# Performance work log

Hardware: AMD Instinct MI355X
Metric: run time of the kernel (lower is better)

The kernel has to match this reference:

```python
import jax, jax.numpy as jnp
import numpy as np

BLOCK_SIZE = 256
EMB = 384
HEAD = 64
B = 256
T = 256

def setup_inputs() -> dict:
    key = jax.random.key(0)
    k1, k2, k3, k4 = jax.random.split(key, 4)
    x = jax.random.normal(k1, (B, T, EMB), dtype=jnp.float32)
    # torch Linear(no bias) default init ~ U(-1/sqrt(in), 1/sqrt(in)); use scaled normal
    s = 1.0 / np.sqrt(EMB)
    Wq = jax.random.normal(k2, (EMB, HEAD), dtype=jnp.float32) * s
    Wk = jax.random.normal(k3, (EMB, HEAD), dtype=jnp.float32) * s
    Wv = jax.random.normal(k4, (EMB, HEAD), dtype=jnp.float32) * s
    return {"x": x, "Wq": Wq, "Wk": Wk, "Wv": Wv}

def reference(x, Wq, Wk, Wv):
    Bb, Tt, C = x.shape
    q = jnp.einsum('btc,ch->bth', x, Wq)
    k = jnp.einsum('btc,ch->bth', x, Wk)
    v = jnp.einsum('btc,ch->bth', x, Wv)
    # NOTE: source scales by C**-0.5 where C = embedding dim (384), not head_size
    scores = jnp.einsum('bth,bsh->bts', q, k) * (C ** -0.5)  # [B,T,T]
    causal = jnp.tril(jnp.ones((Tt, Tt), dtype=bool))
    scores = jnp.where(causal, scores, -jnp.inf)
    weights = jax.nn.softmax(scores, axis=-1)
    # dropout is identity in eval mode (reference baseline)
    out = jnp.einsum('bts,bsh->bth', weights, v)
    return out
```

## Files before the change

kernel.cpp:

```cpp
#include <hip/hip_runtime.h>
#include <hip/hip_bf16.h>
#include <cstdint>
#include <cstddef>

#define B_DIM 256
#define T_DIM 256
#define EMB   384
#define HEAD  64

typedef __attribute__((ext_vector_type(8))) short bf16x8;
typedef __attribute__((ext_vector_type(4))) float f32x4;
typedef __attribute__((ext_vector_type(4))) unsigned int u32x4;

__device__ __forceinline__ unsigned short f2bf(float f) {
    union { float f; unsigned int u; } v; v.f = f;
    unsigned int r = v.u + 0x7fffu + ((v.u >> 16) & 1u);
    return (unsigned short)(r >> 16);
}

__device__ __forceinline__ unsigned int pkbf(float a, float b) {
#if __has_builtin(__builtin_amdgcn_cvt_pk_bf16_f32)
    typedef __attribute__((ext_vector_type(2))) __bf16 bf16x2_t;
    bf16x2_t r = __builtin_amdgcn_cvt_pk_bf16_f32(a, b);
    return *(unsigned int*)&r;
#else
    return (unsigned)f2bf(a) | ((unsigned)f2bf(b) << 16);
#endif
}

__global__ void wprep_kernel(const float* __restrict__ Wq, const float* __restrict__ Wk,
                             const float* __restrict__ Wv, unsigned short* __restrict__ Wb) {
    int g = blockIdx.x * blockDim.x + threadIdx.x;
    if (g >= 9216) return;
    int kkstep = g / 1536, rem = g - kkstep * 1536;
    int r = rem >> 3, cs = rem & 7, c = cs ^ (r & 7);
    const float* W = (r < 64) ? Wq : (r < 128) ? Wk : Wv;
    int h = r & 63;
    unsigned short tmp[8];
#pragma unroll
    for (int e = 0; e < 8; ++e) {
        int k = kkstep * 64 + c * 8 + e;
        tmp[e] = f2bf(W[k * HEAD + h]);
    }
    *(u32x4*)(Wb + (size_t)g * 8) = *(u32x4*)tmp;
}

__global__ __launch_bounds__(512, 2) void fused_kernel(const float* __restrict__ x,
                                                       const unsigned short* __restrict__ Wb,
                                                       float* __restrict__ out) {
    __shared__ union SM {
        struct { unsigned short Xs[2][256][72]; unsigned short Ws[2][12288]; } p1;
        struct { unsigned short qs[256][72]; unsigned short ks[256][72];
                 unsigned short vT[64][264]; unsigned short Ps[8][16][72]; } p2;
    } sm;

    const int tid = threadIdx.x;
    const int w = tid >> 6, lane = tid & 63, qd = lane >> 4, l15 = lane & 15;
    const int mh = w >> 1, nh = w & 1;
    const int b = blockIdx.x;
    const float* xb = x + (size_t)b * T_DIM * EMB;
    const int xrow = tid >> 4, xc4 = (tid & 15) << 2;

    f32x4 acc[4][6];
#pragma unroll
    for (int mt = 0; mt < 4; ++mt)
#pragma unroll
        for (int nt = 0; nt < 6; ++nt) acc[mt][nt] = (f32x4){0.f, 0.f, 0.f, 0.f};

    float4 xr[8];
#pragma unroll
    for (int s = 0; s < 3; ++s) {
        int idx = s * 512 + w * 64;
        const unsigned short* gp = Wb + (size_t)(idx + lane) * 8;
        unsigned short* lp = &sm.p1.Ws[0][idx * 8];
        __builtin_amdgcn_global_load_lds(
            (const __attribute__((address_space(1))) unsigned int*)gp,
            (__attribute__((address_space(3))) unsigned int*)lp, 16, 0, 0);
    }
#pragma unroll
    for (int s = 0; s < 8; ++s)
        xr[s] = *(const float4*)(xb + (size_t)(xrow + 32 * s) * EMB + xc4);
#pragma unroll
    for (int s = 0; s < 8; ++s)
        *(uint2*)&sm.p1.Xs[0][xrow + 32 * s][xc4] = make_uint2(pkbf(xr[s].x, xr[s].y), pkbf(xr[s].z, xr[s].w));

    for (int kk = 0; kk < 6; ++kk) {
        __syncthreads();
        if (kk < 5) {
#pragma unroll
            for (int s = 0; s < 3; ++s) {
                int idx = s * 512 + w * 64;
                const unsigned short* gp = Wb + (size_t)((kk + 1) * 1536 + idx + lane) * 8;
                unsigned short* lp = &sm.p1.Ws[(kk + 1) & 1][idx * 8];
                __builtin_amdgcn_global_load_lds(
                    (const __attribute__((address_space(1))) unsigned int*)gp,
                    (__attribute__((address_space(3))) unsigned int*)lp, 16, 0, 0);
            }
#pragma unroll
            for (int s = 0; s < 8; ++s)
                xr[s] = *(const float4*)(xb + (size_t)(xrow + 32 * s) * EMB + (kk + 1) * 64 + xc4);
        }
#pragma unroll
        for (int kb = 0; kb < 2; ++kb) {
            bf16x8 a[4], bb[6];
#pragma unroll
            for (int mt = 0; mt < 4; ++mt)
                a[mt] = *(const bf16x8*)&sm.p1.Xs[kk & 1][64 * mh + 16 * mt + l15][32 * kb + 8 * qd];
#pragma unroll
            for (int nt = 0; nt < 6; ++nt) {
                int n = 96 * nh + 16 * nt + l15;
                bb[nt] = *(const bf16x8*)&sm.p1.Ws[kk & 1][n * 64 + (((4 * kb + qd) ^ (n & 7)) << 3)];
            }
#pragma unroll
            for (int mt = 0; mt < 4; ++mt)
#pragma unroll
                for (int nt = 0; nt < 6; ++nt)
                    acc[mt][nt] = __builtin_amdgcn_mfma_f32_16x16x32_bf16(a[mt], bb[nt], acc[mt][nt], 0, 0, 0);
        }
        if (kk < 5) {
#pragma unroll
            for (int s = 0; s < 8; ++s)
                *(uint2*)&sm.p1.Xs[(kk + 1) & 1][xrow + 32 * s][xc4] =
                    make_uint2(pkbf(xr[s].x, xr[s].y), pkbf(xr[s].z, xr[s].w));
        }
    }
    __syncthreads();

#pragma unroll
    for (int nt = 0; nt < 6; ++nt) {
        int n = 96 * nh + 16 * nt + l15;
        int arr = n >> 6, h = n & 63;
        if (arr == 2) {
#pragma unroll
            for (int mt = 0; mt < 4; ++mt) {
                int tok0 = 64 * mh + 16 * mt + 4 * qd;
                *(uint2*)&sm.p2.vT[h][tok0] = make_uint2(
                    pkbf(acc[mt][nt][0], acc[mt][nt][1]),
                    pkbf(acc[mt][nt][2], acc[mt][nt][3]));
            }
        } else {
#pragma unroll
            for (int mt = 0; mt < 4; ++mt)
#pragma unroll
                for (int reg = 0; reg < 4; ++reg) {
                    int tok = 64 * mh + 16 * mt + 4 * qd + reg;
                    unsigned short val = f2bf(acc[mt][nt][reg]);
                    if (arr == 0) sm.p2.qs[tok][h] = val;
                    else          sm.p2.ks[tok][h] = val;
                }
        }
    }
    __syncthreads();

    const int tiles[2] = { w, 15 - w };
    bf16x8 aq[2][2];
#pragma unroll
    for (int ti = 0; ti < 2; ++ti)
#pragma unroll
        for (int kbi = 0; kbi < 2; ++kbi)
            aq[ti][kbi] = *(const bf16x8*)&sm.p2.qs[16 * tiles[ti] + l15][32 * kbi + 8 * qd];

    f32x4 O[2][4];
    float l[2][4];
#pragma unroll
    for (int ti = 0; ti < 2; ++ti) {
#pragma unroll
        for (int dn = 0; dn < 4; ++dn) O[ti][dn] = (f32x4){0.f, 0.f, 0.f, 0.f};
#pragma unroll
        for (int reg = 0; reg < 4; ++reg) l[ti][reg] = 0.f;
    }

    const float cExp = 1.4426950408889634f / 19.595917942265423f;

#pragma unroll
    for (int ti = 0; ti < 2; ++ti) {
        const int t = tiles[ti];
        for (int jc = 0; jc <= (t >> 2); ++jc) {
            const int ntmax = min(3, t - 4 * jc);
            f32x4 S[4];
#pragma unroll
            for (int nt = 0; nt < 4; ++nt) {
                if (nt <= ntmax) {
                    bf16x8 b0 = *(const bf16x8*)&sm.p2.ks[64 * jc + 16 * nt + l15][8 * qd];
                    bf16x8 b1 = *(const bf16x8*)&sm.p2.ks[64 * jc + 16 * nt + l15][32 + 8 * qd];
                    f32x4 s = __builtin_amdgcn_mfma_f32_16x16x32_bf16(aq[ti][0], b0, (f32x4){0.f,0.f,0.f,0.f}, 0, 0, 0);
                    s = __builtin_amdgcn_mfma_f32_16x16x32_bf16(aq[ti][1], b1, s, 0, 0, 0);
                    S[nt] = s;
                }
            }
#pragma unroll
            for (int nt = 0; nt < 4; ++nt) {
#pragma unroll
                for (int reg = 0; reg < 4; ++reg) {
                    float p = 0.0f;
                    if (nt <= ntmax) {
                        p = exp2f(S[nt][reg] * cExp);
                        if (4 * jc + nt == t && (l15 > 4 * qd + reg)) p = 0.0f;
                    }
                    l[ti][reg] += p;
                    sm.p2.Ps[w][4 * qd + reg][16 * nt + l15] = f2bf(p);
                }
            }
            bf16x8 ap0 = *(const bf16x8*)&sm.p2.Ps[w][l15][8 * qd];
            bf16x8 ap1 = *(const bf16x8*)&sm.p2.Ps[w][l15][32 + 8 * qd];
#pragma unroll
            for (int dn = 0; dn < 4; ++dn) {
                bf16x8 bv0 = *(const bf16x8*)&sm.p2.vT[16 * dn + l15][64 * jc + 8 * qd];
                bf16x8 bv1 = *(const bf16x8*)&sm.p2.vT[16 * dn + l15][64 * jc + 32 + 8 * qd];
                O[ti][dn] = __builtin_amdgcn_mfma_f32_16x16x32_bf16(ap0, bv0, O[ti][dn], 0, 0, 0);
                O[ti][dn] = __builtin_amdgcn_mfma_f32_16x16x32_bf16(ap1, bv1, O[ti][dn], 0, 0, 0);
            }
        }
    }

#pragma unroll
    for (int ti = 0; ti < 2; ++ti) {
#pragma unroll
        for (int reg = 0; reg < 4; ++reg) {
            float s = l[ti][reg];
            s += __shfl_xor(s, 1);
            s += __shfl_xor(s, 2);
            s += __shfl_xor(s, 4);
            s += __shfl_xor(s, 8);
            float inv = 1.0f / s;
            int row = 16 * tiles[ti] + 4 * qd + reg;
            float* dst = out + ((size_t)b * T_DIM + row) * HEAD;
#pragma unroll
            for (int dn = 0; dn < 4; ++dn)
                dst[16 * dn + l15] = O[ti][dn][reg] * inv;
        }
    }
}

extern "C" void kernel_launch(void* const* d_in, const int* in_sizes, int n_in,
                              void* d_out, int out_size, void* d_ws, size_t ws_size,
                              hipStream_t stream) {
    const float* x  = (const float*)d_in[0];
    const float* Wq = (const float*)d_in[1];
    const float* Wk = (const float*)d_in[2];
    const float* Wv = (const float*)d_in[3];
    float* out = (float*)d_out;

    unsigned short* Wb = (unsigned short*)d_ws;

    wprep_kernel<<<36, 256, 0, stream>>>(Wq, Wk, Wv, Wb);
    fused_kernel<<<B_DIM, 512, 0, stream>>>(x, Wb, out);
}
```

Measured before the change: 170.9 us.

## Prefetch entire x row into registers upfront and scatter chunks to LDS per step

Each thread now owns half of one token row. It loads its full 192-float slice of x up front with a 3-deep rolling register buffer, converts it to packed bf16 held in 96 registers, and writes each 64-column chunk into the LDS double buffer just before it is needed. This front-loads all global x traffic and removes the per-iteration global loads from the projection loop. The cost is a large jump in register use under launch_bounds(512,2), which risks spills. Half the threads also sit idle during each scatter step.

```diff
diff --git a/kernel.cpp b/kernel.cpp
--- a/kernel.cpp
+++ b/kernel.cpp
@@ -59,15 +59,8 @@
     const int mh = w >> 1, nh = w & 1;
     const int b = blockIdx.x;
     const float* xb = x + (size_t)b * T_DIM * EMB;
-    const int xrow = tid >> 4, xc4 = (tid & 15) << 2;
-
-    f32x4 acc[4][6];
-#pragma unroll
-    for (int mt = 0; mt < 4; ++mt)
-#pragma unroll
-        for (int nt = 0; nt < 6; ++nt) acc[mt][nt] = (f32x4){0.f, 0.f, 0.f, 0.f};
-
-    float4 xr[8];
+    const int r = tid >> 1, h = tid & 1;
+
 #pragma unroll
     for (int s = 0; s < 3; ++s) {
         int idx = s * 512 + w * 64;
@@ -77,13 +70,52 @@
             (const __attribute__((address_space(1))) unsigned int*)gp,
             (__attribute__((address_space(3))) unsigned int*)lp, 16, 0, 0);
     }
-#pragma unroll
-    for (int s = 0; s < 8; ++s)
-        xr[s] = *(const float4*)(xb + (size_t)(xrow + 32 * s) * EMB + xc4);
-#pragma unroll
-    for (int s = 0; s < 8; ++s)
-        *(uint2*)&sm.p1.Xs[0][xrow + 32 * s][xc4] = make_uint2(pkbf(xr[s].x, xr[s].y), pkbf(xr[s].z, xr[s].w));
-
+
+    const float* xp = xb + (size_t)r * EMB + h * 64;
+    float4 xf[3][8];
+    unsigned int st0[32], st1[32], st2[32];
+
+#define LOADC(BUF, C) do { \
+    _Pragma("unroll") \
+    for (int ii = 0; ii < 8; ++ii) \
+        xf[BUF][ii] = *(const float4*)(xp + ((C) >> 1) * 128 + ((C) & 1) * 32 + ii * 4); \
+} while (0)
+
+#define CONVC(BUF, ST, C) do { \
+    _Pragma("unroll") \
+    for (int ii = 0; ii < 8; ++ii) { \
+        ST[16 * ((C) & 1) + 2 * ii]     = pkbf(xf[BUF][ii].x, xf[BUF][ii].y); \
+        ST[16 * ((C) & 1) + 2 * ii + 1] = pkbf(xf[BUF][ii].z, xf[BUF][ii].w); \
+    } \
+} while (0)
+
+    LOADC(0, 0); LOADC(1, 1); LOADC(2, 2);
+    CONVC(0, st0, 0); LOADC(0, 3);
+    CONVC(1, st0, 1); LOADC(1, 4);
+    CONVC(2, st1, 2); LOADC(2, 5);
+    CONVC(0, st1, 3);
+    CONVC(1, st2, 4);
+    CONVC(2, st2, 5);
+
+#define SCATTER(ST, S) do { \
+    if (h == ((S) & 1)) { \
+        _Pragma("unroll") \
+        for (int q = 0; q < 8; ++q) \
+            *(u32x4*)&sm.p1.Xs[(S) & 1][r][8 * q] = \
+                (u32x4){ST[4 * q], ST[4 * q + 1], ST[4 * q + 2], ST[4 * q + 3]}; \
+    } \
+} while (0)
+
+    SCATTER(st0, 0);
+    SCATTER(st0, 1);
+
+    f32x4 acc[4][6];
+#pragma unroll
+    for (int mt = 0; mt < 4; ++mt)
+#pragma unroll
+        for (int nt = 0; nt < 6; ++nt) acc[mt][nt] = (f32x4){0.f, 0.f, 0.f, 0.f};
+
+#pragma unroll
     for (int kk = 0; kk < 6; ++kk) {
         __syncthreads();
         if (kk < 5) {
@@ -96,9 +128,6 @@
                     (const __attribute__((address_space(1))) unsigned int*)gp,
                     (__attribute__((address_space(3))) unsigned int*)lp, 16, 0, 0);
             }
-#pragma unroll
-            for (int s = 0; s < 8; ++s)
-                xr[s] = *(const float4*)(xb + (size_t)(xrow + 32 * s) * EMB + (kk + 1) * 64 + xc4);
         }
 #pragma unroll
         for (int kb = 0; kb < 2; ++kb) {
@@ -117,24 +146,22 @@
                 for (int nt = 0; nt < 6; ++nt)
                     acc[mt][nt] = __builtin_amdgcn_mfma_f32_16x16x32_bf16(a[mt], bb[nt], acc[mt][nt], 0, 0, 0);
         }
-        if (kk < 5) {
-#pragma unroll
-            for (int s = 0; s < 8; ++s)
-                *(uint2*)&sm.p1.Xs[(kk + 1) & 1][xrow + 32 * s][xc4] =
-                    make_uint2(pkbf(xr[s].x, xr[s].y), pkbf(xr[s].z, xr[s].w));
-        }
+        if (kk == 1) SCATTER(st1, 2);
+        if (kk == 2) SCATTER(st1, 3);
+        if (kk == 3) SCATTER(st2, 4);
+        if (kk == 4) SCATTER(st2, 5);
     }
     __syncthreads();
 
 #pragma unroll
     for (int nt = 0; nt < 6; ++nt) {
         int n = 96 * nh + 16 * nt + l15;
-        int arr = n >> 6, h = n & 63;
+        int arr = n >> 6, hh = n & 63;
         if (arr == 2) {
 #pragma unroll
             for (int mt = 0; mt < 4; ++mt) {
                 int tok0 = 64 * mh + 16 * mt + 4 * qd;
-                *(uint2*)&sm.p2.vT[h][tok0] = make_uint2(
+                *(uint2*)&sm.p2.vT[hh][tok0] = make_uint2(
                     pkbf(acc[mt][nt][0], acc[mt][nt][1]),
                     pkbf(acc[mt][nt][2], acc[mt][nt][3]));
             }
@@ -145,8 +172,8 @@
                 for (int reg = 0; reg < 4; ++reg) {
                     int tok = 64 * mh + 16 * mt + 4 * qd + reg;
                     unsigned short val = f2bf(acc[mt][nt][reg]);
-                    if (arr == 0) sm.p2.qs[tok][h] = val;
-                    else          sm.p2.ks[tok][h] = val;
+                    if (arr == 0) sm.p2.qs[tok][hh] = val;
+                    else          sm.p2.ks[tok][hh] = val;
                 }
         }
     }
```

New measurement: 183.0 us. 1.07x slower.

## Split fused attention into separate QKV projection and attention kernels

Applied to the files above, without the earlier changes.

Replaces the single per-batch fused kernel (512 threads, one block per batch) with a QKV projection kernel and an attention kernel. Each runs 512 blocks of 256 threads, with each block handling half the tokens. Q, K and V go through global workspace in bf16 using XOR-swizzled layouts, and the LDS tiles drop their padding in favour of swizzles. The goal is more blocks for better occupancy and load balance across CUs. The cost is an extra global round trip for Q/K/V, a second kernel launch, and reloading the full K/V in every attention block.

```diff
diff --git a/kernel.cpp b/kernel.cpp
--- a/kernel.cpp
+++ b/kernel.cpp
@@ -27,6 +27,10 @@
     return (unsigned)f2bf(a) | ((unsigned)f2bf(b) << 16);
 #endif
 }
+
+#define WS_Q_OFF  (1u  << 20)
+#define WS_K_OFF  (16u << 20)
+#define WS_V_OFF  (32u << 20)
 
 __global__ void wprep_kernel(const float* __restrict__ Wq, const float* __restrict__ Wk,
                              const float* __restrict__ Wv, unsigned short* __restrict__ Wb) {
@@ -45,21 +49,56 @@
     *(u32x4*)(Wb + (size_t)g * 8) = *(u32x4*)tmp;
 }
 
-__global__ __launch_bounds__(512, 2) void fused_kernel(const float* __restrict__ x,
-                                                       const unsigned short* __restrict__ Wb,
-                                                       float* __restrict__ out) {
+__global__ __launch_bounds__(256) void qkv_kernel(const float* __restrict__ x,
+                                                  const unsigned short* __restrict__ Wb,
+                                                  unsigned short* __restrict__ qg,
+                                                  unsigned short* __restrict__ kg,
+                                                  unsigned short* __restrict__ vg) {
     __shared__ union SM {
-        struct { unsigned short Xs[2][256][72]; unsigned short Ws[2][12288]; } p1;
-        struct { unsigned short qs[256][72]; unsigned short ks[256][72];
-                 unsigned short vT[64][264]; unsigned short Ps[8][16][72]; } p2;
+        struct { unsigned short Xs[2][128][64]; unsigned short Ws[2][12288]; } p1;
+        struct { unsigned short qb[128][64]; unsigned short kb[128][64];
+                 unsigned short vTb[64][128]; } p2;
     } sm;
 
     const int tid = threadIdx.x;
     const int w = tid >> 6, lane = tid & 63, qd = lane >> 4, l15 = lane & 15;
     const int mh = w >> 1, nh = w & 1;
-    const int b = blockIdx.x;
-    const float* xb = x + (size_t)b * T_DIM * EMB;
-    const int xrow = tid >> 4, xc4 = (tid & 15) << 2;
+    const int b = blockIdx.x >> 1, p = blockIdx.x & 1;
+    const float* xb = x + ((size_t)b * T_DIM + p * 128) * EMB;
+    const int xrow = tid >> 4, fc = tid & 15;
+
+#define WGLDS(KSTEP, BUF) do { \
+    _Pragma("unroll") \
+    for (int s = 0; s < 6; ++s) { \
+        int idx = s * 256 + w * 64; \
+        const unsigned short* gp = Wb + (size_t)((KSTEP) * 1536 + idx + lane) * 8; \
+        unsigned short* lp = &sm.p1.Ws[BUF][idx * 8]; \
+        __builtin_amdgcn_global_load_lds( \
+            (const __attribute__((address_space(1))) unsigned int*)gp, \
+            (__attribute__((address_space(3))) unsigned int*)lp, 16, 0, 0); \
+    } \
+} while (0)
+
+#define XLOAD(KK) do { \
+    _Pragma("unroll") \
+    for (int s = 0; s < 8; ++s) \
+        xr[s] = *(const float4*)(xb + (size_t)(xrow + 16 * s) * EMB + (KK) * 64 + 4 * fc); \
+} while (0)
+
+#define XWRITE(BUF) do { \
+    _Pragma("unroll") \
+    for (int s = 0; s < 8; ++s) { \
+        int row_ = xrow + 16 * s; \
+        *(uint2*)((char*)&sm.p1.Xs[BUF][0][0] + row_ * 128 + \
+                  ((((fc >> 1) ^ (row_ & 7)) << 4) | ((fc & 1) << 3))) = \
+            make_uint2(pkbf(xr[s].x, xr[s].y), pkbf(xr[s].z, xr[s].w)); \
+    } \
+} while (0)
+
+    float4 xr[8];
+    WGLDS(0, 0);
+    XLOAD(0);
+    XWRITE(0);
 
     f32x4 acc[4][6];
 #pragma unroll
@@ -67,45 +106,22 @@
 #pragma unroll
         for (int nt = 0; nt < 6; ++nt) acc[mt][nt] = (f32x4){0.f, 0.f, 0.f, 0.f};
 
-    float4 xr[8];
-#pragma unroll
-    for (int s = 0; s < 3; ++s) {
-        int idx = s * 512 + w * 64;
-        const unsigned short* gp = Wb + (size_t)(idx + lane) * 8;
-        unsigned short* lp = &sm.p1.Ws[0][idx * 8];
-        __builtin_amdgcn_global_load_lds(
-            (const __attribute__((address_space(1))) unsigned int*)gp,
-            (__attribute__((address_space(3))) unsigned int*)lp, 16, 0, 0);
-    }
-#pragma unroll
-    for (int s = 0; s < 8; ++s)
-        xr[s] = *(const float4*)(xb + (size_t)(xrow + 32 * s) * EMB + xc4);
-#pragma unroll
-    for (int s = 0; s < 8; ++s)
-        *(uint2*)&sm.p1.Xs[0][xrow + 32 * s][xc4] = make_uint2(pkbf(xr[s].x, xr[s].y), pkbf(xr[s].z, xr[s].w));
-
+#pragma unroll
     for (int kk = 0; kk < 6; ++kk) {
         __syncthreads();
         if (kk < 5) {
-#pragma unroll
-            for (int s = 0; s < 3; ++s) {
-                int idx = s * 512 + w * 64;
-                const unsigned short* gp = Wb + (size_t)((kk + 1) * 1536 + idx + lane) * 8;
-                unsigned short* lp = &sm.p1.Ws[(kk + 1) & 1][idx * 8];
-                __builtin_amdgcn_global_load_lds(
-                    (const __attribute__((address_space(1))) unsigned int*)gp,
-                    (__attribute__((address_space(3))) unsigned int*)lp, 16, 0, 0);
-            }
-#pragma unroll
-            for (int s = 0; s < 8; ++s)
-                xr[s] = *(const float4*)(xb + (size_t)(xrow + 32 * s) * EMB + (kk + 1) * 64 + xc4);
+            WGLDS(kk + 1, (kk + 1) & 1);
+            XLOAD(kk + 1);
         }
 #pragma unroll
         for (int kb = 0; kb < 2; ++kb) {
             bf16x8 a[4], bb[6];
 #pragma unroll
-            for (int mt = 0; mt < 4; ++mt)
-                a[mt] = *(const bf16x8*)&sm.p1.Xs[kk & 1][64 * mh + 16 * mt + l15][32 * kb + 8 * qd];
+            for (int mt = 0; mt < 4; ++mt) {
+                int rl = 64 * mh + 16 * mt + l15;
+                a[mt] = *(const bf16x8*)((const char*)&sm.p1.Xs[kk & 1][0][0] +
+                                         rl * 128 + ((((kb << 2) + qd) ^ (rl & 7)) << 4));
+            }
 #pragma unroll
             for (int nt = 0; nt < 6; ++nt) {
                 int n = 96 * nh + 16 * nt + l15;
@@ -117,48 +133,99 @@
                 for (int nt = 0; nt < 6; ++nt)
                     acc[mt][nt] = __builtin_amdgcn_mfma_f32_16x16x32_bf16(a[mt], bb[nt], acc[mt][nt], 0, 0, 0);
         }
-        if (kk < 5) {
-#pragma unroll
-            for (int s = 0; s < 8; ++s)
-                *(uint2*)&sm.p1.Xs[(kk + 1) & 1][xrow + 32 * s][xc4] =
-                    make_uint2(pkbf(xr[s].x, xr[s].y), pkbf(xr[s].z, xr[s].w));
-        }
+        if (kk < 5) XWRITE((kk + 1) & 1);
     }
     __syncthreads();
 
 #pragma unroll
     for (int nt = 0; nt < 6; ++nt) {
         int n = 96 * nh + 16 * nt + l15;
-        int arr = n >> 6, h = n & 63;
+        int arr = n >> 6, hh = n & 63;
         if (arr == 2) {
 #pragma unroll
             for (int mt = 0; mt < 4; ++mt) {
                 int tok0 = 64 * mh + 16 * mt + 4 * qd;
-                *(uint2*)&sm.p2.vT[h][tok0] = make_uint2(
+                *(uint2*)&sm.p2.vTb[hh][tok0] = make_uint2(
                     pkbf(acc[mt][nt][0], acc[mt][nt][1]),
                     pkbf(acc[mt][nt][2], acc[mt][nt][3]));
             }
         } else {
+            char* base = (arr == 0) ? (char*)&sm.p2.qb[0][0] : (char*)&sm.p2.kb[0][0];
 #pragma unroll
             for (int mt = 0; mt < 4; ++mt)
 #pragma unroll
                 for (int reg = 0; reg < 4; ++reg) {
                     int tok = 64 * mh + 16 * mt + 4 * qd + reg;
-                    unsigned short val = f2bf(acc[mt][nt][reg]);
-                    if (arr == 0) sm.p2.qs[tok][h] = val;
-                    else          sm.p2.ks[tok][h] = val;
+                    *(unsigned short*)(base + tok * 128 +
+                        ((((hh >> 3) ^ (tok & 7)) << 4) | ((hh & 7) << 1))) = f2bf(acc[mt][nt][reg]);
                 }
         }
     }
     __syncthreads();
 
-    const int tiles[2] = { w, 15 - w };
+    {
+        int row = tid >> 1, cb = (tid & 1) * 4;
+        size_t gq = (size_t)b * 32768 + (p * 128 + row) * 128;
+#pragma unroll
+        for (int i = 0; i < 4; ++i) {
+            *(u32x4*)((char*)qg + gq + (cb + i) * 16) =
+                *(const u32x4*)((const char*)&sm.p2.qb[0][0] + row * 128 + (cb + i) * 16);
+            *(u32x4*)((char*)kg + gq + (cb + i) * 16) =
+                *(const u32x4*)((const char*)&sm.p2.kb[0][0] + row * 128 + (cb + i) * 16);
+        }
+        int ch = tid >> 2, cg = (tid & 3) * 4;
+#pragma unroll
+        for (int i = 0; i < 4; ++i) {
+            int cl = cg + i;
+            u32x4 v = *(const u32x4*)((const char*)&sm.p2.vTb[0][0] + ch * 256 + cl * 16);
+            *(u32x4*)((char*)vg + (size_t)b * 32768 + ch * 512 + p * 256 +
+                      ((cl & 8) << 4) + (((cl & 7) ^ (ch & 7)) << 4)) = v;
+        }
+    }
+}
+
+__global__ __launch_bounds__(256) void attn_kernel(const unsigned short* __restrict__ qg,
+                                                   const unsigned short* __restrict__ kg,
+                                                   const unsigned short* __restrict__ vg,
+                                                   float* __restrict__ out) {
+    __shared__ struct {
+        unsigned short ks[256][64];
+        unsigned short vT[64][256];
+        unsigned short Ps[4][16][72];
+    } sm;
+
+    const int tid = threadIdx.x;
+    const int w = tid >> 6, lane = tid & 63, qd = lane >> 4, l15 = lane & 15;
+    const int b = blockIdx.x >> 1, p = blockIdx.x & 1;
+
+#pragma unroll
+    for (int s = 0; s < 8; ++s) {
+        int idx = s * 256 + w * 64;
+        __builtin_amdgcn_global_load_lds(
+            (const __attribute__((address_space(1))) unsigned int*)(kg + (size_t)b * 16384 + (idx + lane) * 8),
+            (__attribute__((address_space(3))) unsigned int*)(&sm.ks[0][0] + idx * 8), 16, 0, 0);
+    }
+#pragma unroll
+    for (int s = 0; s < 8; ++s) {
+        int idx = s * 256 + w * 64;
+        __builtin_amdgcn_global_load_lds(
+            (const __attribute__((address_space(1))) unsigned int*)(vg + (size_t)b * 16384 + (idx + lane) * 8),
+            (__attribute__((address_space(3))) unsigned int*)(&sm.vT[0][0] + idx * 8), 16, 0, 0);
+    }
+
+    const int tiles[2] = { 2 * w + p, 14 - 2 * w + p };
+
     bf16x8 aq[2][2];
 #pragma unroll
     for (int ti = 0; ti < 2; ++ti)
 #pragma unroll
-        for (int kbi = 0; kbi < 2; ++kbi)
-            aq[ti][kbi] = *(const bf16x8*)&sm.p2.qs[16 * tiles[ti] + l15][32 * kbi + 8 * qd];
+        for (int kbi = 0; kbi < 2; ++kbi) {
+            int row = 16 * tiles[ti] + l15;
+            aq[ti][kbi] = *(const bf16x8*)((const char*)qg + (size_t)b * 32768 + row * 128 +
+                                           ((((kbi << 2) + qd) ^ (l15 & 7)) << 4));
+        }
+
+    __syncthreads();
 
     f32x4 O[2][4];
     float l[2][4];
@@ -181,8 +248,11 @@
 #pragma unroll
             for (int nt = 0; nt < 4; ++nt) {
                 if (nt <= ntmax) {
-                    bf16x8 b0 = *(const bf16x8*)&sm.p2.ks[64 * jc + 16 * nt + l15][8 * qd];
-                    bf16x8 b1 = *(const bf16x8*)&sm.p2.ks[64 * jc + 16 * nt + l15][32 + 8 * qd];
+                    int rk = 64 * jc + 16 * nt + l15;
+                    bf16x8 b0 = *(const bf16x8*)((const char*)&sm.ks[0][0] + rk * 128 +
+                                                 ((qd ^ (l15 & 7)) << 4));
+                    bf16x8 b1 = *(const bf16x8*)((const char*)&sm.ks[0][0] + rk * 128 +
+                                                 (((4 + qd) ^ (l15 & 7)) << 4));
                     f32x4 s = __builtin_amdgcn_mfma_f32_16x16x32_bf16(aq[ti][0], b0, (f32x4){0.f,0.f,0.f,0.f}, 0, 0, 0);
                     s = __builtin_amdgcn_mfma_f32_16x16x32_bf16(aq[ti][1], b1, s, 0, 0, 0);
                     S[nt] = s;
@@ -192,21 +262,24 @@
             for (int nt = 0; nt < 4; ++nt) {
 #pragma unroll
                 for (int reg = 0; reg < 4; ++reg) {
-                    float p = 0.0f;
+                    float pv = 0.0f;
                     if (nt <= ntmax) {
-                        p = exp2f(S[nt][reg] * cExp);
-                        if (4 * jc + nt == t && (l15 > 4 * qd + reg)) p = 0.0f;
+                        pv = exp2f(S[nt][reg] * cExp);
+                        if (4 * jc + nt == t && (l15 > 4 * qd + reg)) pv = 0.0f;
                     }
-                    l[ti][reg] += p;
-                    sm.p2.Ps[w][4 * qd + reg][16 * nt + l15] = f2bf(p);
+                    l[ti][reg] += pv;
+                    sm.Ps[w][4 * qd + reg][16 * nt + l15] = f2bf(pv);
                 }
             }
-            bf16x8 ap0 = *(const bf16x8*)&sm.p2.Ps[w][l15][8 * qd];
-            bf16x8 ap1 = *(const bf16x8*)&sm.p2.Ps[w][l15][32 + 8 * qd];
+            bf16x8 ap0 = *(const bf16x8*)&sm.Ps[w][l15][8 * qd];
+            bf16x8 ap1 = *(const bf16x8*)&sm.Ps[w][l15][32 + 8 * qd];
 #pragma unroll
             for (int dn = 0; dn < 4; ++dn) {
-                bf16x8 bv0 = *(const bf16x8*)&sm.p2.vT[16 * dn + l15][64 * jc + 8 * qd];
-                bf16x8 bv1 = *(const bf16x8*)&sm.p2.vT[16 * dn + l15][64 * jc + 32 + 8 * qd];
+                int rv = 16 * dn + l15;
+                bf16x8 bv0 = *(const bf16x8*)((const char*)&sm.vT[0][0] + rv * 512 +
+                                              ((8 * jc + (qd ^ (l15 & 7))) << 4));
+                bf16x8 bv1 = *(const bf16x8*)((const char*)&sm.vT[0][0] + rv * 512 +
+                                              ((8 * jc + ((4 + qd) ^ (l15 & 7))) << 4));
                 O[ti][dn] = __builtin_amdgcn_mfma_f32_16x16x32_bf16(ap0, bv0, O[ti][dn], 0, 0, 0);
                 O[ti][dn] = __builtin_amdgcn_mfma_f32_16x16x32_bf16(ap1, bv1, O[ti][dn], 0, 0, 0);
             }
@@ -242,7 +315,11 @@
     float* out = (float*)d_out;
 
     unsigned short* Wb = (unsigned short*)d_ws;
+    unsigned short* qg = (unsigned short*)((char*)d_ws + WS_Q_OFF);
+    unsigned short* kg = (unsigned short*)((char*)d_ws + WS_K_OFF);
+    unsigned short* vg = (unsigned short*)((char*)d_ws + WS_V_OFF);
 
     wprep_kernel<<<36, 256, 0, stream>>>(Wq, Wk, Wv, Wb);
-    fused_kernel<<<B_DIM, 512, 0, stream>>>(x, Wb, out);
-}
+    qkv_kernel<<<2 * B_DIM, 256, 0, stream>>>(x, Wb, qg, kg, vg);
+    attn_kernel<<<2 * B_DIM, 256, 0, stream>>>(qg, kg, vg, out);
+}
```

New measurement: 183.8 us. 1.08x slower.
